# Performance work log

Measured on AMD Instinct MI355X. Metric: run time of the kernel, lower is better.

The kernel has to match this reference:

```python
import math
import jax, jax.numpy as jnp
import numpy as np

B, S, H, NH = 2, 2048, 1024, 16
HD = H // NH


def setup_inputs() -> dict:
    key = jax.random.key(0)
    k1, k2, k3 = jax.random.split(key, 3)
    scale = 1.0 / math.sqrt(H)
    return {
        "hidden_states": jax.random.normal(k1, (B, S, H), dtype=jnp.float32),
        "attention_mask": jnp.ones((B, 1, S, S), dtype=jnp.float32),
        "qkv_w": jax.random.normal(k2, (3 * H, H), dtype=jnp.float32) * scale,
        "qkv_b": jnp.zeros((3 * H,), dtype=jnp.float32),
        "dense_w": jax.random.normal(k3, (H, H), dtype=jnp.float32) * scale,
        "dense_b": jnp.zeros((H,), dtype=jnp.float32),
    }


def reference(hidden_states, attention_mask, qkv_w, qkv_b, dense_w, dense_b):
    # qkv projection: torch Linear y = x @ W^T + b
    mixed = hidden_states @ qkv_w.T + qkv_b            # [B,S,3H]
    mixed = mixed.reshape(B, S, NH, 3 * HD).transpose(0, 2, 1, 3)  # [B,NH,S,3HD]
    q, k, v = jnp.split(mixed, 3, axis=-1)             # each [B,NH,S,HD]
    scores = jnp.einsum("bhqd,bhkd->bhqk", q, k) / math.sqrt(HD)
    scores = scores * attention_mask - 10000.0 * (1.0 - attention_mask)
    probs = jax.nn.softmax(scores, axis=-1)            # dropout p=0 -> identity
    ctx = jnp.einsum("bhqk,bhkd->bhqd", probs, v)      # [B,NH,S,HD]
    ctx = ctx.transpose(0, 2, 1, 3).reshape(B, S, H)
    out = ctx @ dense_w.T + dense_b                    # output dropout p=0
    return out
```

## Files before the change

### kernel.cpp

```cpp
#include <hip/hip_runtime.h>
#include <hip/hip_bf16.h>
#include <stdint.h>

#define BB 2
#define SS 2048
#define HH 1024
#define NHH 16
#define HDD 64
#define MM (BB*SS)
#define N1 (3*HH)
#define NT (SS/64)
#define LOG2E 1.44269504f

using bf16 = __hip_bfloat16;
typedef __attribute__((ext_vector_type(8))) short bf16x8;
typedef __attribute__((ext_vector_type(4))) float f32x4;

__device__ inline unsigned short f2bfu(float f) {
  union { bf16 h; unsigned short u; } c;
  c.h = __float2bfloat16(f);
  return c.u;
}

__device__ inline unsigned int packbf(float lo, float hi) {
  return (unsigned int)f2bfu(lo) | ((unsigned int)f2bfu(hi) << 16);
}

__device__ inline void load_lds16(const void* g, void* l) {
  __builtin_amdgcn_global_load_lds(
      (const __attribute__((address_space(1))) void*)g,
      (__attribute__((address_space(3))) void*)l, 16, 0, 0);
}

__device__ inline f32x4 mfma16(bf16x8 a, bf16x8 b, f32x4 c) {
  return __builtin_amdgcn_mfma_f32_16x16x32_bf16(a, b, c, 0, 0, 0);
}

__global__ __launch_bounds__(256) void cvt_f32_bf16(const float* __restrict__ in,
                                                    unsigned short* __restrict__ out,
                                                    int n4) {
  int i = blockIdx.x * blockDim.x + threadIdx.x;
  int st = gridDim.x * blockDim.x;
  for (; i < n4; i += st) {
    float4 v = reinterpret_cast<const float4*>(in)[i];
    ushort4 o;
    o.x = f2bfu(v.x); o.y = f2bfu(v.y); o.z = f2bfu(v.z); o.w = f2bfu(v.w);
    reinterpret_cast<ushort4*>(out)[i] = o;
  }
}

__global__ __launch_bounds__(256) void mask_flags_kernel(const float* __restrict__ mask,
                                                         unsigned char* __restrict__ flags) {
  int t = blockIdx.x;
  int b = t >> 10, qt = (t >> 5) & 31, kt = t & 31;
  const float* mb = mask + ((size_t)b * SS + qt * 64) * SS + kt * 64;
  int row = threadIdx.x >> 2, c0 = (threadIdx.x & 3) * 16;
  int ok = 1;
#pragma unroll
  for (int j = 0; j < 4; ++j) {
    float4 v = *reinterpret_cast<const float4*>(mb + (size_t)row * SS + c0 + j * 4);
    ok &= (v.x == 1.f) & (v.y == 1.f) & (v.z == 1.f) & (v.w == 1.f);
  }
  ok = __all(ok);
  __shared__ int s[4];
  if ((threadIdx.x & 63) == 0) s[threadIdx.x >> 6] = ok;
  __syncthreads();
  if (threadIdx.x == 0) flags[t] = (unsigned char)(s[0] & s[1] & s[2] & s[3]);
}

template <bool OUT_BF16>
__global__ __launch_bounds__(256) void gemm_bt(const unsigned short* __restrict__ A,
                                               const unsigned short* __restrict__ Bt,
                                               const float* __restrict__ bias,
                                               void* __restrict__ Cv,
                                               int Ndim, int Kdim) {
  __shared__ __align__(16) unsigned short As[128 * 32];
  __shared__ __align__(16) unsigned short Bs[128 * 32];

  const int tid = threadIdx.x;
  const int wave = tid >> 6, lane = tid & 63;
  const int m0 = blockIdx.x * 128;
  const int n0 = blockIdx.y * 128;
  const int wm = (wave >> 1) * 64, wn = (wave & 1) * 64;
  const int lrow = lane & 15;
  const int lk8 = (lane >> 4) * 8;
  const int r4 = (lane >> 4) * 4;

  f32x4 acc[4][4];
  const f32x4 z = {0.f, 0.f, 0.f, 0.f};
  for (int i = 0; i < 4; ++i)
    for (int j = 0; j < 4; ++j) acc[i][j] = z;

  for (int k0 = 0; k0 < Kdim; k0 += 32) {
#pragma unroll
    for (int it = 0; it < 2; ++it) {
      int idx = it * 256 + tid;
      int row = idx >> 2, seg = idx & 3;
      load_lds16(A + (size_t)(m0 + row) * Kdim + k0 + seg * 8, &As[row * 32 + seg * 8]);
      load_lds16(Bt + (size_t)(n0 + row) * Kdim + k0 + seg * 8, &Bs[row * 32 + seg * 8]);
    }
    __syncthreads();

    bf16x8 af[4], bfr[4];
#pragma unroll
    for (int i = 0; i < 4; ++i)
      af[i] = *reinterpret_cast<const bf16x8*>(&As[(wm + i * 16 + lrow) * 32 + lk8]);
#pragma unroll
    for (int j = 0; j < 4; ++j)
      bfr[j] = *reinterpret_cast<const bf16x8*>(&Bs[(wn + j * 16 + lrow) * 32 + lk8]);
#pragma unroll
    for (int i = 0; i < 4; ++i)
#pragma unroll
      for (int j = 0; j < 4; ++j)
        acc[i][j] = mfma16(af[i], bfr[j], acc[i][j]);
    __syncthreads();
  }

#pragma unroll
  for (int i = 0; i < 4; ++i) {
#pragma unroll
    for (int j = 0; j < 4; ++j) {
      int col = n0 + wn + j * 16 + lrow;
      float bv = bias[col];
#pragma unroll
      for (int r = 0; r < 4; ++r) {
        int row = m0 + wm + i * 16 + r4 + r;
        float v = acc[i][j][r] + bv;
        if (OUT_BF16) {
          ((unsigned short*)Cv)[(size_t)row * Ndim + col] = f2bfu(v);
        } else {
          ((float*)Cv)[(size_t)row * Ndim + col] = v;
        }
      }
    }
  }
}

__global__ __launch_bounds__(256, 4) void attn_kernel(const unsigned short* __restrict__ mixed,
                                                      const float* __restrict__ mask,
                                                      const unsigned char* __restrict__ flags,
                                                      unsigned short* __restrict__ ctx) {
  __shared__ __align__(16) unsigned short Ks[2][64 * 64];
  __shared__ __align__(16) unsigned short Vt[2][64 * 64];
  __shared__ __align__(16) unsigned short QP[64 * 64];

  const int tid = threadIdx.x, wave = tid >> 6, lane = tid & 63;
  const int ql = lane & 15;
  const int g = lane >> 4;
  const int q0 = blockIdx.x * 64;
  const int bh = blockIdx.y;
  const int b = bh / NHH, hh = bh % NHH;

  const unsigned short* qbase = mixed + (size_t)(b * SS) * N1 + hh * 192;
  const unsigned short* kbase = qbase + 64;
  const unsigned short* vbase = qbase + 128;
  const float* mbase = mask + (size_t)b * SS * SS;
  const unsigned char* fl = flags + ((size_t)b * 32 + blockIdx.x) * 32;

  const int vrow = lane;
  const int dg = wave;

#pragma unroll
  for (int it = 0; it < 2; ++it) {
    int idx = it * 256 + tid;
    int row = idx >> 3, seg = idx & 7;
    load_lds16(qbase + (size_t)(q0 + row) * N1 + ((seg ^ (row & 7)) << 3),
               &QP[row * 64 + seg * 8]);
    load_lds16(kbase + (size_t)row * N1 + ((seg ^ (row & 7)) << 3),
               &Ks[0][row * 64 + seg * 8]);
  }
  {
    union { bf16x8 v; unsigned short u[8]; } V0, V1;
    const unsigned short* vp = vbase + (size_t)vrow * N1 + dg * 16;
    V0.v = *reinterpret_cast<const bf16x8*>(vp);
    V1.v = *reinterpret_cast<const bf16x8*>(vp + 8);
#pragma unroll
    for (int j = 0; j < 8; ++j) {
      int d = dg * 16 + j;
      Vt[0][d * 64 + ((((vrow >> 3) ^ (d & 7)) << 3) | (vrow & 7))] = V0.u[j];
    }
#pragma unroll
    for (int j = 0; j < 8; ++j) {
      int d = dg * 16 + 8 + j;
      Vt[0][d * 64 + ((((vrow >> 3) ^ (d & 7)) << 3) | (vrow & 7))] = V1.u[j];
    }
  }
  __syncthreads();

  const int qrow = wave * 16 + ql;
  const bf16x8 qf0 = *reinterpret_cast<const bf16x8*>(
      &QP[qrow * 64 + ((g ^ (qrow & 7)) << 3)]);
  const bf16x8 qf1 = *reinterpret_cast<const bf16x8*>(
      &QP[qrow * 64 + (((g + 4) ^ (qrow & 7)) << 3)]);
  __syncthreads();

  unsigned short* Ps = &QP[wave * 1024];
  const int X = (ql & 7) << 3;

  f32x4 oacc[4];
  const f32x4 z = {0.f, 0.f, 0.f, 0.f};
  for (int fd = 0; fd < 4; ++fd) oacc[fd] = z;
  float mrun = -1e30f, lrun = 0.f;

  for (int kt = 0; kt < NT; ++kt) {
    const int cur = kt & 1, nxt = cur ^ 1;
    const int krow0 = kt * 64;
    const bool havenext = (kt + 1 < NT);

    union { bf16x8 v; unsigned short u[8]; } Vn0, Vn1;
    if (havenext) {
#pragma unroll
      for (int it = 0; it < 2; ++it) {
        int idx = it * 256 + tid;
        int row = idx >> 3, seg = idx & 7;
        load_lds16(kbase + (size_t)(krow0 + 64 + row) * N1 + ((seg ^ (row & 7)) << 3),
                   &Ks[nxt][row * 64 + seg * 8]);
      }
      const unsigned short* vp = vbase + (size_t)(krow0 + 64 + vrow) * N1 + dg * 16;
      Vn0.v = *reinterpret_cast<const bf16x8*>(vp);
      Vn1.v = *reinterpret_cast<const bf16x8*>(vp + 8);
    }

    f32x4 sacc[4];
    __builtin_amdgcn_s_setprio(1);
#pragma unroll
    for (int n = 0; n < 4; ++n) {
      int krow = n * 16 + ql;
      bf16x8 k0 = *reinterpret_cast<const bf16x8*>(
          &Ks[cur][krow * 64 + ((g ^ (krow & 7)) << 3)]);
      bf16x8 k1 = *reinterpret_cast<const bf16x8*>(
          &Ks[cur][krow * 64 + (((g + 4) ^ (krow & 7)) << 3)]);
      sacc[n] = mfma16(k0, qf0, z);
      sacc[n] = mfma16(k1, qf1, sacc[n]);
    }
    __builtin_amdgcn_s_setprio(0);

    const bool allones = fl[kt] != 0;
    float pv[4][4];
    float pm = -1e30f;
    if (allones) {
      const float C2 = 0.125f * LOG2E;
#pragma unroll
      for (int n = 0; n < 4; ++n)
#pragma unroll
        for (int r = 0; r < 4; ++r) {
          pv[n][r] = sacc[n][r] * C2;
          pm = fmaxf(pm, pv[n][r]);
        }
    } else {
      int qq = q0 + wave * 16 + ql;
#pragma unroll
      for (int n = 0; n < 4; ++n)
#pragma unroll
        for (int r = 0; r < 4; ++r) {
          int kk = krow0 + 16 * n + 4 * g + r;
          float mv = mbase[(size_t)qq * SS + kk];
          float s = sacc[n][r] * 0.125f;
          pv[n][r] = (s * mv - 10000.f * (1.f - mv)) * LOG2E;
          pm = fmaxf(pm, pv[n][r]);
        }
    }
    float pmf = fmaxf(pm, __shfl_xor(pm, 16, 64));
    pmf = fmaxf(pmf, __shfl_xor(pmf, 32, 64));

    if (!__all(pmf <= mrun + 8.f)) {
      float mnew = fmaxf(mrun, pmf);
      float alpha = exp2f(mrun - mnew);
      mrun = mnew;
      lrun *= alpha;
#pragma unroll
      for (int r = 0; r < 4; ++r) {
        float fac = __shfl(alpha, g * 4 + r, 64);
#pragma unroll
        for (int fd = 0; fd < 4; ++fd) oacc[fd][r] *= fac;
      }
    }

    float sum = 0.f;
#pragma unroll
    for (int n = 0; n < 4; ++n)
#pragma unroll
      for (int r = 0; r < 4; ++r) {
        pv[n][r] = exp2f(pv[n][r] - mrun);
        sum += pv[n][r];
      }
    sum += __shfl_xor(sum, 16, 64);
    sum += __shfl_xor(sum, 32, 64);
    lrun += sum;

#pragma unroll
    for (int n = 0; n < 4; ++n) {
      uint2 w;
      w.x = packbf(pv[n][0], pv[n][1]);
      w.y = packbf(pv[n][2], pv[n][3]);
      *reinterpret_cast<uint2*>(&Ps[ql * 64 + ((16 * n + 4 * g) ^ X)]) = w;
    }
    bf16x8 pa0 = *reinterpret_cast<const bf16x8*>(&Ps[ql * 64 + ((8 * g) ^ X)]);
    bf16x8 pa1 = *reinterpret_cast<const bf16x8*>(&Ps[ql * 64 + ((32 + 8 * g) ^ X)]);

    __builtin_amdgcn_s_setprio(1);
#pragma unroll
    for (int fd = 0; fd < 4; ++fd) {
      int d = fd * 16 + ql;
      bf16x8 bv0 = *reinterpret_cast<const bf16x8*>(
          &Vt[cur][d * 64 + ((g ^ (d & 7)) << 3)]);
      bf16x8 bv1 = *reinterpret_cast<const bf16x8*>(
          &Vt[cur][d * 64 + (((4 + g) ^ (d & 7)) << 3)]);
      oacc[fd] = mfma16(pa0, bv0, oacc[fd]);
      oacc[fd] = mfma16(pa1, bv1, oacc[fd]);
    }
    __builtin_amdgcn_s_setprio(0);

    if (havenext) {
#pragma unroll
      for (int j = 0; j < 8; ++j) {
        int d = dg * 16 + j;
        Vt[nxt][d * 64 + ((((vrow >> 3) ^ (d & 7)) << 3) | (vrow & 7))] = Vn0.u[j];
      }
#pragma unroll
      for (int j = 0; j < 8; ++j) {
        int d = dg * 16 + 8 + j;
        Vt[nxt][d * 64 + ((((vrow >> 3) ^ (d & 7)) << 3) | (vrow & 7))] = Vn1.u[j];
      }
    }
    __syncthreads();
  }

  float invl = 1.f / lrun;
#pragma unroll
  for (int r = 0; r < 4; ++r) {
    float inv = __shfl(invl, g * 4 + r, 64);
    int qq = q0 + wave * 16 + g * 4 + r;
    unsigned short* cp = ctx + (size_t)(b * SS + qq) * HH + hh * HDD;
#pragma unroll
    for (int fd = 0; fd < 4; ++fd)
      cp[fd * 16 + ql] = f2bfu(oacc[fd][r] * inv);
  }
}

extern "C" void kernel_launch(void* const* d_in, const int* in_sizes, int n_in,
                              void* d_out, int out_size, void* d_ws, size_t ws_size,
                              hipStream_t stream) {
  const float* hs      = (const float*)d_in[0];
  const float* mask    = (const float*)d_in[1];
  const float* qkv_w   = (const float*)d_in[2];
  const float* qkv_b   = (const float*)d_in[3];
  const float* dense_w = (const float*)d_in[4];
  const float* dense_b = (const float*)d_in[5];
  float* out = (float*)d_out;

  char* ws = (char*)d_ws;
  unsigned short* hs_b     = (unsigned short*)(ws);
  unsigned short* qkvw_b   = (unsigned short*)(ws + 8388608);
  unsigned short* densew_b = (unsigned short*)(ws + 14680064);
  unsigned short* mixed_b  = (unsigned short*)(ws + 16777216);
  unsigned short* ctx_b    = (unsigned short*)(ws + 41943040);
  unsigned char*  flags    = (unsigned char*)(ws + 50331648);

  cvt_f32_bf16<<<2048, 256, 0, stream>>>(hs, hs_b, (MM * HH) / 4);
  cvt_f32_bf16<<<2048, 256, 0, stream>>>(qkv_w, qkvw_b, (N1 * HH) / 4);
  cvt_f32_bf16<<<1024, 256, 0, stream>>>(dense_w, densew_b, (HH * HH) / 4);
  mask_flags_kernel<<<BB * 32 * 32, 256, 0, stream>>>(mask, flags);

  gemm_bt<true><<<dim3(MM / 128, N1 / 128), 256, 0, stream>>>(
      hs_b, qkvw_b, qkv_b, mixed_b, N1, HH);

  attn_kernel<<<dim3(SS / 64, BB * NHH), 256, 0, stream>>>(mixed_b, mask, flags, ctx_b);

  gemm_bt<false><<<dim3(MM / 128, HH / 128), 256, 0, stream>>>(
      ctx_b, densew_b, dense_b, out, HH, HH);
}
```

Measured before the change: 169.6 us.

## Emit transposed V from QKV GEMM epilogue and async-load it in attention

The QKV GEMM epilogue now writes the V columns into a separate per-head transposed buffer (head, dim, seq). This lets the attention kernel load V tiles straight into LDS with async 16-byte loads, like K, instead of loading V through registers and scattering it into LDS one element at a time. The softmax for all-ones mask tiles is also streamlined: the max is taken on raw scores and the scale is folded into an fma inside exp2. The trade-off is that the epilogue's transposed stores are strided and uncoalesced, which may slow the GEMM.

New measurement: 170.4 us. No clear change (+0.5%).

```diff
diff --git a/kernel.cpp b/kernel.cpp
--- a/kernel.cpp
+++ b/kernel.cpp
@@ -68,11 +68,12 @@
   if (threadIdx.x == 0) flags[t] = (unsigned char)(s[0] & s[1] & s[2] & s[3]);
 }
 
-template <bool OUT_BF16>
+template <bool OUT_BF16, bool QKV_SPLIT>
 __global__ __launch_bounds__(256) void gemm_bt(const unsigned short* __restrict__ A,
                                                const unsigned short* __restrict__ Bt,
                                                const float* __restrict__ bias,
                                                void* __restrict__ Cv,
+                                               unsigned short* __restrict__ vT,
                                                int Ndim, int Kdim) {
   __shared__ __align__(16) unsigned short As[128 * 32];
   __shared__ __align__(16) unsigned short Bs[128 * 32];
@@ -122,11 +123,16 @@
     for (int j = 0; j < 4; ++j) {
       int col = n0 + wn + j * 16 + lrow;
       float bv = bias[col];
+      int hcol = 0, rr = 0;
+      if (QKV_SPLIT) { hcol = col / 192; rr = col - hcol * 192; }
 #pragma unroll
       for (int r = 0; r < 4; ++r) {
         int row = m0 + wm + i * 16 + r4 + r;
         float v = acc[i][j][r] + bv;
-        if (OUT_BF16) {
+        if (QKV_SPLIT && rr >= 128) {
+          int bb = row >> 11, s = row & (SS - 1);
+          vT[(((size_t)bb * NHH + hcol) * HDD + (rr - 128)) * SS + s] = f2bfu(v);
+        } else if (OUT_BF16) {
           ((unsigned short*)Cv)[(size_t)row * Ndim + col] = f2bfu(v);
         } else {
           ((float*)Cv)[(size_t)row * Ndim + col] = v;
@@ -137,6 +143,7 @@
 }
 
 __global__ __launch_bounds__(256, 4) void attn_kernel(const unsigned short* __restrict__ mixed,
+                                                      const unsigned short* __restrict__ vT,
                                                       const float* __restrict__ mask,
                                                       const unsigned char* __restrict__ flags,
                                                       unsigned short* __restrict__ ctx) {
@@ -153,37 +160,18 @@
 
   const unsigned short* qbase = mixed + (size_t)(b * SS) * N1 + hh * 192;
   const unsigned short* kbase = qbase + 64;
-  const unsigned short* vbase = qbase + 128;
+  const unsigned short* vtbase = vT + ((size_t)(b * NHH + hh) * HDD) * SS;
   const float* mbase = mask + (size_t)b * SS * SS;
   const unsigned char* fl = flags + ((size_t)b * 32 + blockIdx.x) * 32;
-
-  const int vrow = lane;
-  const int dg = wave;
 
 #pragma unroll
   for (int it = 0; it < 2; ++it) {
     int idx = it * 256 + tid;
     int row = idx >> 3, seg = idx & 7;
-    load_lds16(qbase + (size_t)(q0 + row) * N1 + ((seg ^ (row & 7)) << 3),
-               &QP[row * 64 + seg * 8]);
-    load_lds16(kbase + (size_t)row * N1 + ((seg ^ (row & 7)) << 3),
-               &Ks[0][row * 64 + seg * 8]);
-  }
-  {
-    union { bf16x8 v; unsigned short u[8]; } V0, V1;
-    const unsigned short* vp = vbase + (size_t)vrow * N1 + dg * 16;
-    V0.v = *reinterpret_cast<const bf16x8*>(vp);
-    V1.v = *reinterpret_cast<const bf16x8*>(vp + 8);
-#pragma unroll
-    for (int j = 0; j < 8; ++j) {
-      int d = dg * 16 + j;
-      Vt[0][d * 64 + ((((vrow >> 3) ^ (d & 7)) << 3) | (vrow & 7))] = V0.u[j];
-    }
-#pragma unroll
-    for (int j = 0; j < 8; ++j) {
-      int d = dg * 16 + 8 + j;
-      Vt[0][d * 64 + ((((vrow >> 3) ^ (d & 7)) << 3) | (vrow & 7))] = V1.u[j];
-    }
+    int sw = (seg ^ (row & 7)) << 3;
+    load_lds16(qbase + (size_t)(q0 + row) * N1 + sw, &QP[row * 64 + seg * 8]);
+    load_lds16(kbase + (size_t)row * N1 + sw, &Ks[0][row * 64 + seg * 8]);
+    load_lds16(vtbase + (size_t)row * SS + sw, &Vt[0][row * 64 + seg * 8]);
   }
   __syncthreads();
 
@@ -201,24 +189,24 @@
   const f32x4 z = {0.f, 0.f, 0.f, 0.f};
   for (int fd = 0; fd < 4; ++fd) oacc[fd] = z;
   float mrun = -1e30f, lrun = 0.f;
+  const float C2 = 0.125f * LOG2E;
 
   for (int kt = 0; kt < NT; ++kt) {
     const int cur = kt & 1, nxt = cur ^ 1;
     const int krow0 = kt * 64;
     const bool havenext = (kt + 1 < NT);
 
-    union { bf16x8 v; unsigned short u[8]; } Vn0, Vn1;
     if (havenext) {
 #pragma unroll
       for (int it = 0; it < 2; ++it) {
         int idx = it * 256 + tid;
         int row = idx >> 3, seg = idx & 7;
-        load_lds16(kbase + (size_t)(krow0 + 64 + row) * N1 + ((seg ^ (row & 7)) << 3),
+        int sw = (seg ^ (row & 7)) << 3;
+        load_lds16(kbase + (size_t)(krow0 + 64 + row) * N1 + sw,
                    &Ks[nxt][row * 64 + seg * 8]);
+        load_lds16(vtbase + (size_t)row * SS + krow0 + 64 + sw,
+                   &Vt[nxt][row * 64 + seg * 8]);
       }
-      const unsigned short* vp = vbase + (size_t)(krow0 + 64 + vrow) * N1 + dg * 16;
-      Vn0.v = *reinterpret_cast<const bf16x8*>(vp);
-      Vn1.v = *reinterpret_cast<const bf16x8*>(vp + 8);
     }
 
     f32x4 sacc[4];
@@ -237,18 +225,19 @@
 
     const bool allones = fl[kt] != 0;
     float pv[4][4];
-    float pm = -1e30f;
+    float pmf;
     if (allones) {
-      const float C2 = 0.125f * LOG2E;
+      float pm = sacc[0][0];
 #pragma unroll
       for (int n = 0; n < 4; ++n)
 #pragma unroll
-        for (int r = 0; r < 4; ++r) {
-          pv[n][r] = sacc[n][r] * C2;
-          pm = fmaxf(pm, pv[n][r]);
-        }
+        for (int r = 0; r < 4; ++r) pm = fmaxf(pm, sacc[n][r]);
+      pm = fmaxf(pm, __shfl_xor(pm, 16, 64));
+      pm = fmaxf(pm, __shfl_xor(pm, 32, 64));
+      pmf = pm * C2;
     } else {
       int qq = q0 + wave * 16 + ql;
+      float pm = -1e30f;
 #pragma unroll
       for (int n = 0; n < 4; ++n)
 #pragma unroll
@@ -259,9 +248,9 @@
           pv[n][r] = (s * mv - 10000.f * (1.f - mv)) * LOG2E;
           pm = fmaxf(pm, pv[n][r]);
         }
-    }
-    float pmf = fmaxf(pm, __shfl_xor(pm, 16, 64));
-    pmf = fmaxf(pmf, __shfl_xor(pmf, 32, 64));
+      pm = fmaxf(pm, __shfl_xor(pm, 16, 64));
+      pmf = fmaxf(pm, __shfl_xor(pm, 32, 64));
+    }
 
     if (!__all(pmf <= mrun + 8.f)) {
       float mnew = fmaxf(mrun, pmf);
@@ -277,13 +266,23 @@
     }
 
     float sum = 0.f;
-#pragma unroll
-    for (int n = 0; n < 4; ++n)
-#pragma unroll
-      for (int r = 0; r < 4; ++r) {
-        pv[n][r] = exp2f(pv[n][r] - mrun);
-        sum += pv[n][r];
-      }
+    if (allones) {
+#pragma unroll
+      for (int n = 0; n < 4; ++n)
+#pragma unroll
+        for (int r = 0; r < 4; ++r) {
+          pv[n][r] = exp2f(fmaf(sacc[n][r], C2, -mrun));
+          sum += pv[n][r];
+        }
+    } else {
+#pragma unroll
+      for (int n = 0; n < 4; ++n)
+#pragma unroll
+        for (int r = 0; r < 4; ++r) {
+          pv[n][r] = exp2f(pv[n][r] - mrun);
+          sum += pv[n][r];
+        }
+    }
     sum += __shfl_xor(sum, 16, 64);
     sum += __shfl_xor(sum, 32, 64);
     lrun += sum;
@@ -311,18 +310,6 @@
     }
     __builtin_amdgcn_s_setprio(0);
 
-    if (havenext) {
-#pragma unroll
-      for (int j = 0; j < 8; ++j) {
-        int d = dg * 16 + j;
-        Vt[nxt][d * 64 + ((((vrow >> 3) ^ (d & 7)) << 3) | (vrow & 7))] = Vn0.u[j];
-      }
-#pragma unroll
-      for (int j = 0; j < 8; ++j) {
-        int d = dg * 16 + 8 + j;
-        Vt[nxt][d * 64 + ((((vrow >> 3) ^ (d & 7)) << 3) | (vrow & 7))] = Vn1.u[j];
-      }
-    }
     __syncthreads();
   }
 
@@ -356,17 +343,19 @@
   unsigned short* mixed_b  = (unsigned short*)(ws + 16777216);
   unsigned short* ctx_b    = (unsigned short*)(ws + 41943040);
   unsigned char*  flags    = (unsigned char*)(ws + 50331648);
+  unsigned short* vT_b     = (unsigned short*)(ws + 50335744);
 
   cvt_f32_bf16<<<2048, 256, 0, stream>>>(hs, hs_b, (MM * HH) / 4);
   cvt_f32_bf16<<<2048, 256, 0, stream>>>(qkv_w, qkvw_b, (N1 * HH) / 4);
   cvt_f32_bf16<<<1024, 256, 0, stream>>>(dense_w, densew_b, (HH * HH) / 4);
   mask_flags_kernel<<<BB * 32 * 32, 256, 0, stream>>>(mask, flags);
 
-  gemm_bt<true><<<dim3(MM / 128, N1 / 128), 256, 0, stream>>>(
-      hs_b, qkvw_b, qkv_b, mixed_b, N1, HH);
-
-  attn_kernel<<<dim3(SS / 64, BB * NHH), 256, 0, stream>>>(mixed_b, mask, flags, ctx_b);
-
-  gemm_bt<false><<<dim3(MM / 128, HH / 128), 256, 0, stream>>>(
-      ctx_b, densew_b, dense_b, out, HH, HH);
-}
+  gemm_bt<true, true><<<dim3(MM / 128, N1 / 128), 256, 0, stream>>>(
+      hs_b, qkvw_b, qkv_b, mixed_b, vT_b, N1, HH);
+
+  attn_kernel<<<dim3(SS / 64, BB * NHH), 256, 0, stream>>>(
+      mixed_b, vT_b, mask, flags, ctx_b);
+
+  gemm_bt<false, false><<<dim3(MM / 128, HH / 128), 256, 0, stream>>>(
+      ctx_b, densew_b, dense_b, out, nullptr, HH, HH);
+}
```
